# Kernel tuning notes

Measured on AMD Instinct MI355X. Metric: run time of the kernel, lower is better.

## Reference

```python
import jax, jax.numpy as jnp
import numpy as np


def _hard_sigmoid(x):
    # Keras ConvLSTM2D default recurrent_activation
    return jnp.clip(0.2 * x + 0.5, 0.0, 1.0)


def _conv_same(x, w):
    # x: [B,H,W,Cin], w: [kh,kw,Cin,Cout]
    return jax.lax.conv_general_dilated(
        x, w, window_strides=(1, 1), padding='SAME',
        dimension_numbers=('NHWC', 'HWIO', 'NHWC'))


def setup_inputs() -> dict:
    key = jax.random.key(0)
    ks = jax.random.split(key, 6)
    B, T, H, W, F = 16, 16, 64, 64, 64
    return {
        'inputs': jax.random.normal(ks[0], (B, T, H, W, 1), jnp.float32),  # only T is used
        'h0': jax.random.normal(ks[1], (B, H, W, F), jnp.float32),
        'c0': jax.random.normal(ks[2], (B, H, W, F), jnp.float32),
        'kernels': jax.random.normal(ks[3], (T, 3, 3, F, 4 * F), jnp.float32) * 0.05,
        'rec_kernels': jax.random.normal(ks[4], (T, 3, 3, F, 4 * F), jnp.float32) * 0.05,
        'bias': jnp.zeros((T, 4 * F), jnp.float32),
    }


def reference(inputs, h0, c0, kernels, rec_kernels, bias):
    # The layer feeds h back as the cell input each step, so the cell input x == h.
    # By linearity, conv(h, Wk) + conv(h, Uk) == conv(h, Wk + Uk); we fuse the two convs.
    # Gate order (Keras ConvLSTM2DCell): i, f, c, o.
    def step(carry, params):
        h, c = carry
        Wk, Uk, b = params  # [3,3,F,4F], [3,3,F,4F], [4F]
        z = _conv_same(h, Wk + Uk) + b  # [B,H,W,4F]
        zi, zf, zc, zo = jnp.split(z, 4, axis=-1)
        i = _hard_sigmoid(zi)
        f = _hard_sigmoid(zf)
        c_new = f * c + i * jnp.tanh(zc)
        o = _hard_sigmoid(zo)
        h_new = o * jnp.tanh(c_new)
        return (h_new, c_new), h_new

    (_, _), hs = jax.lax.scan(step, (h0, c0), (kernels, rec_kernels, bias))
    return jnp.moveaxis(hs, 0, 1)  # [B, T, H, W, F]
```

## Files before the change

### kernel.cpp

```cpp
#include <hip/hip_runtime.h>
#include <math.h>

typedef _Float16 f16;
typedef _Float16 f16x4 __attribute__((ext_vector_type(4)));
typedef _Float16 f16x8 __attribute__((ext_vector_type(8)));
typedef float f32x4 __attribute__((ext_vector_type(4)));

#define NB 16
#define NT 16
#define NH 64
#define NW 64
#define NF 64
#define NG 256
#define HWF ((size_t)NH * NW * NF)
#define OUT_BSTRIDE ((size_t)NT * HWF)
#define RS2 8448
#define WSTEP ((size_t)18432)

#define MFMA(a, b, c) __builtin_amdgcn_mfma_f32_16x16x32_f16((a), (b), (c), 0, 0, 0)

__device__ __forceinline__ void gload_lds16(const void* g, void* l) {
    __builtin_amdgcn_global_load_lds(
        (const __attribute__((address_space(1))) unsigned int*)(g),
        (__attribute__((address_space(3))) unsigned int*)(l), 16, 0, 0);
}

__device__ __forceinline__ float hsig(float x) {
    return fminf(fmaxf(0.2f * x + 0.5f, 0.0f), 1.0f);
}

__device__ __forceinline__ float ftanh(float x) {
    float t = __builtin_amdgcn_exp2f(x * 2.885390081777927f);
    return 1.0f - 2.0f * __builtin_amdgcn_rcpf(t + 1.0f);
}

__global__ void fuse_w_hi(const float* __restrict__ k, const float* __restrict__ rk,
                          f16* __restrict__ wf2) {
    int idx = blockIdx.x * 256 + threadIdx.x;
    if (idx >= NT * 9 * NG * 8) return;
    int g8   = idx & 7;
    int cout = (idx >> 3) & 255;
    int tt   = idx >> 11;
    int tap  = tt % 9;
    int t    = tt / 9;
    int kk = g8 >> 2, lg = g8 & 3;

    const float* ks = k  + (size_t)tt * NF * NG + cout;
    const float* rs = rk + (size_t)tt * NF * NG + cout;

    f16 hi8[8];
#pragma unroll
    for (int j = 0; j < 8; ++j) {
        int cin = kk * 32 + lg * 8 + j;
        hi8[j] = (f16)(ks[(size_t)cin * NG] + rs[(size_t)cin * NG]);
    }
    const int lane = lg * 16 + (cout & 15);
    const int cb   = ((cout >> 4) & 3) * 4 + (cout >> 6);
    size_t chunk = (size_t)t * WSTEP + (size_t)(tap * 2 + kk) * 1024 +
                   (size_t)cb * 64 + lane;
    *(f16x8*)&wf2[chunk * 8] = *(f16x8*)hi8;
}

__global__ void f32_to_f16(const float* __restrict__ src, f16* __restrict__ dst, int n4) {
    int i = blockIdx.x * 256 + threadIdx.x;
    if (i >= n4) return;
    float4 v = ((const float4*)src)[i];
    f16x4 o = { (f16)v.x, (f16)v.y, (f16)v.z, (f16)v.w };
    *(f16x4*)&dst[(size_t)i * 4] = o;
}

__global__ void __launch_bounds__(512, 4)
convlstm_mfma_step(const f16* __restrict__ h2in, f16* __restrict__ h2out,
                   f16* __restrict__ cbuf,
                   float* __restrict__ hout,
                   const f16* __restrict__ wt,
                   const float* __restrict__ bias)
{
    __shared__ __align__(16) unsigned char lds[4 * RS2];

    const int tid  = threadIdx.x;
    const int w    = tid >> 6;
    const int lane = tid & 63;

    const int id = blockIdx.x;
    const int bb = ((id & 7) << 1) + ((id >> 8) & 1);
    const int y0 = ((id >> 3) & 31) * 2;

    const int wm = w >> 2;
    const int wn = w & 3;
    const int lm = lane & 15;
    const int lg = lane >> 4;

    const f16x8* wb = (const f16x8*)wt + (size_t)(wn * 4) * 64 + lane;
    f16x8 bh[4];
#pragma unroll
    for (int nf = 0; nf < 4; ++nf)
        bh[nf] = wb[nf * 64];

    if (tid < 64) {
        int row = tid >> 4, side = (tid >> 3) & 1, j = tid & 7;
        *(f16x8*)&lds[row * RS2 + side * (65 * 128) + j * 16] = (f16x8)(_Float16)0.0f;
    }

    {
        const int r    = w >> 1;
        const int gy   = y0 - 1 + r;
        const int half = w & 1;
        const unsigned dbase = r * RS2 + 128 + half * 4096;
        if (gy >= 0 && gy < NH) {
            const unsigned char* gsrc = (const unsigned char*)h2in +
                ((((size_t)bb * NH + gy) * NW) << 7);
#pragma unroll
            for (int i = 0; i < 4; ++i) {
                const int xrel = half * 32 + i * 8 + (lane >> 3);
                const unsigned src = ((unsigned)xrel << 7) +
                    ((unsigned)((lane & 7) ^ ((xrel + 1) & 7)) << 4);
                gload_lds16(gsrc + src, (void*)&lds[dbase + i * 1024]);
            }
        } else {
            const f16x8 zf = (f16x8)(_Float16)0.0f;
#pragma unroll
            for (int i = 0; i < 4; ++i)
                *(f16x8*)&lds[dbase + i * 1024 + lane * 16] = zf;
        }
    }
    __syncthreads();

    f32x4 acc[4][4];
#pragma unroll
    for (int mf = 0; mf < 4; ++mf)
#pragma unroll
        for (int nf = 0; nf < 4; ++nf) acc[mf][nf] = (f32x4)0.0f;

    unsigned av[3][2];
#pragma unroll
    for (int d = 0; d < 3; ++d)
#pragma unroll
        for (int kk = 0; kk < 2; ++kk) {
            const int tx = lm + d;
            av[d][kk] = (unsigned)(tx * 128 +
                        (((kk * 4 + lg) ^ (tx & 7)) << 4));
        }

#pragma unroll
    for (int it = 0; it < 18; ++it) {
        if (it > 0) {
#pragma unroll
            for (int nf = 0; nf < 4; ++nf)
                bh[nf] = wb[(size_t)it * 1024 + nf * 64];
        }
        const int tap = it >> 1, kk = it & 1;
        const int ty = tap / 3;
        const int d  = tap - ty * 3;
        const unsigned abase = (unsigned)((wm + ty) * RS2) + av[d][kk];
        __builtin_amdgcn_s_setprio(1);
#pragma unroll
        for (int mf = 0; mf < 4; ++mf) {
            const f16x8 ah = *(const f16x8*)&lds[abase + mf * 2048];
#pragma unroll
            for (int nf = 0; nf < 4; ++nf)
                acc[mf][nf] = MFMA(ah, bh[nf], acc[mf][nf]);
        }
        __builtin_amdgcn_s_setprio(0);
    }

    const int f  = wn * 16 + lm;
    const int gy = y0 + wm;
    const float b0 = bias[f], b1 = bias[64 + f], b2 = bias[128 + f], b3 = bias[192 + f];

#pragma unroll
    for (int mf = 0; mf < 4; ++mf) {
        const int xb = mf * 16 + lg * 4;
        const size_t base = ((((size_t)bb * NH + gy) * NW + xb) << 6) + f;
        f16 cp4[4];
#pragma unroll
        for (int j = 0; j < 4; ++j)
            cp4[j] = cbuf[base + (size_t)j * 64];
#pragma unroll
        for (int j = 0; j < 4; ++j) {
            const float zi  = acc[mf][0][j] + b0;
            const float zfv = acc[mf][1][j] + b1;
            const float zc  = acc[mf][2][j] + b2;
            const float zo  = acc[mf][3][j] + b3;
            const float ig = hsig(zi), fg = hsig(zfv), og = hsig(zo);
            const float cn = fg * (float)cp4[j] + ig * ftanh(zc);
            cbuf[base + (size_t)j * 64] = (f16)cn;
            const float hn = og * ftanh(cn);
            hout[(size_t)bb * OUT_BSTRIDE + (((size_t)gy * NW + xb + j) << 6) + f] = hn;
            h2out[base + (size_t)j * 64] = (f16)hn;
        }
    }
}

extern "C" void kernel_launch(void* const* d_in, const int* in_sizes, int n_in,
                              void* d_out, int out_size, void* d_ws, size_t ws_size,
                              hipStream_t stream) {
    const float* h0    = (const float*)d_in[1];
    const float* c0    = (const float*)d_in[2];
    const float* kern  = (const float*)d_in[3];
    const float* rkern = (const float*)d_in[4];
    const float* bias  = (const float*)d_in[5];
    float* out = (float*)d_out;

    f16* wf2   = (f16*)d_ws;
    f16* h2a   = wf2 + (size_t)NT * WSTEP * 8;
    f16* h2b   = h2a + (size_t)NB * HWF;
    f16* cbuf  = h2b + (size_t)NB * HWF;

    const int n4 = (int)(NB * HWF / 4);
    fuse_w_hi<<<(NT * 9 * NG * 8 + 255) / 256, 256, 0, stream>>>(kern, rkern, wf2);
    f32_to_f16<<<(n4 + 255) / 256, 256, 0, stream>>>(h0, h2a, n4);
    f32_to_f16<<<(n4 + 255) / 256, 256, 0, stream>>>(c0, cbuf, n4);

    for (int t = 0; t < NT; ++t) {
        const f16* hin = (t & 1) ? h2b : h2a;
        f16* hnx       = (t & 1) ? h2a : h2b;
        convlstm_mfma_step<<<dim3(512), 512, 0, stream>>>(
            hin, hnx, cbuf,
            out + (size_t)t * HWF,
            wf2 + (size_t)t * WSTEP * 8,
            bias + t * NG);
    }
}
```

Measured before the change: 384.3 us.

## Enlarge block tile to four output rows and prefetch cell state early

Each block now computes four image rows instead of two, so each wave handles 8 M-fragments and reuses every loaded weight fragment across twice as many MFMAs. This halves the grid to 256 blocks, which reduces weight reloads and halo overhead (6 LDS rows per 4 outputs instead of 4 per 2). The cell-state values are loaded at kernel start so their latency overlaps the convolution. In exchange register pressure roughly doubles (launch bounds drop to 2 waves/SIMD), and the 256-block grid gives fewer blocks than before to spread across the CUs.

```diff
diff --git a/kernel.cpp b/kernel.cpp
--- a/kernel.cpp
+++ b/kernel.cpp
@@ -69,22 +69,22 @@
     *(f16x4*)&dst[(size_t)i * 4] = o;
 }
 
-__global__ void __launch_bounds__(512, 4)
+__global__ void __launch_bounds__(512, 2)
 convlstm_mfma_step(const f16* __restrict__ h2in, f16* __restrict__ h2out,
                    f16* __restrict__ cbuf,
                    float* __restrict__ hout,
                    const f16* __restrict__ wt,
                    const float* __restrict__ bias)
 {
-    __shared__ __align__(16) unsigned char lds[4 * RS2];
+    __shared__ __align__(16) unsigned char lds[6 * RS2];
 
     const int tid  = threadIdx.x;
     const int w    = tid >> 6;
     const int lane = tid & 63;
 
     const int id = blockIdx.x;
-    const int bb = ((id & 7) << 1) + ((id >> 8) & 1);
-    const int y0 = ((id >> 3) & 31) * 2;
+    const int bb = ((id & 7) << 1) + ((id >> 7) & 1);
+    const int y0 = ((id >> 3) & 15) * 4;
 
     const int wm = w >> 2;
     const int wn = w & 3;
@@ -97,38 +97,46 @@
     for (int nf = 0; nf < 4; ++nf)
         bh[nf] = wb[nf * 64];
 
-    if (tid < 64) {
+    const int f = wn * 16 + lm;
+    f16 cp[8][4];
+#pragma unroll
+    for (int mf = 0; mf < 8; ++mf) {
+        const int gy = y0 + wm * 2 + (mf >> 2);
+        const int xb = (mf & 3) * 16 + lg * 4;
+        const size_t base = ((((size_t)bb * NH + gy) * NW + xb) << 6) + f;
+#pragma unroll
+        for (int j = 0; j < 4; ++j)
+            cp[mf][j] = cbuf[base + (size_t)j * 64];
+    }
+
+    if (tid < 96) {
         int row = tid >> 4, side = (tid >> 3) & 1, j = tid & 7;
         *(f16x8*)&lds[row * RS2 + side * (65 * 128) + j * 16] = (f16x8)(_Float16)0.0f;
     }
 
     {
-        const int r    = w >> 1;
-        const int gy   = y0 - 1 + r;
-        const int half = w & 1;
-        const unsigned dbase = r * RS2 + 128 + half * 4096;
-        if (gy >= 0 && gy < NH) {
-            const unsigned char* gsrc = (const unsigned char*)h2in +
-                ((((size_t)bb * NH + gy) * NW) << 7);
-#pragma unroll
-            for (int i = 0; i < 4; ++i) {
-                const int xrel = half * 32 + i * 8 + (lane >> 3);
-                const unsigned src = ((unsigned)xrel << 7) +
-                    ((unsigned)((lane & 7) ^ ((xrel + 1) & 7)) << 4);
-                gload_lds16(gsrc + src, (void*)&lds[dbase + i * 1024]);
+        const int x = w * 8 + (lane >> 3);
+        const int g = lane & 7;
+        const unsigned src = ((unsigned)x << 7) +
+                             ((unsigned)(g ^ ((x + 1) & 7)) << 4);
+#pragma unroll
+        for (int k = 0; k < 6; ++k) {
+            const int gy = y0 - 1 + k;
+            const unsigned dbase = k * RS2 + 128 + w * 1024;
+            if (gy >= 0 && gy < NH) {
+                const unsigned char* gsrc = (const unsigned char*)h2in +
+                    ((((size_t)bb * NH + gy) * NW) << 7);
+                gload_lds16(gsrc + src, (void*)&lds[dbase]);
+            } else {
+                *(f16x8*)&lds[dbase + lane * 16] = (f16x8)(_Float16)0.0f;
             }
-        } else {
-            const f16x8 zf = (f16x8)(_Float16)0.0f;
-#pragma unroll
-            for (int i = 0; i < 4; ++i)
-                *(f16x8*)&lds[dbase + i * 1024 + lane * 16] = zf;
         }
     }
     __syncthreads();
 
-    f32x4 acc[4][4];
-#pragma unroll
-    for (int mf = 0; mf < 4; ++mf)
+    f32x4 acc[8][4];
+#pragma unroll
+    for (int mf = 0; mf < 8; ++mf)
 #pragma unroll
         for (int nf = 0; nf < 4; ++nf) acc[mf][nf] = (f32x4)0.0f;
 
@@ -152,11 +160,12 @@
         const int tap = it >> 1, kk = it & 1;
         const int ty = tap / 3;
         const int d  = tap - ty * 3;
-        const unsigned abase = (unsigned)((wm + ty) * RS2) + av[d][kk];
+        const unsigned abase = (unsigned)((wm * 2 + ty) * RS2) + av[d][kk];
         __builtin_amdgcn_s_setprio(1);
 #pragma unroll
-        for (int mf = 0; mf < 4; ++mf) {
-            const f16x8 ah = *(const f16x8*)&lds[abase + mf * 2048];
+        for (int mf = 0; mf < 8; ++mf) {
+            const f16x8 ah = *(const f16x8*)&lds[abase + (mf >> 2) * RS2 +
+                                                 (mf & 3) * 2048];
 #pragma unroll
             for (int nf = 0; nf < 4; ++nf)
                 acc[mf][nf] = MFMA(ah, bh[nf], acc[mf][nf]);
@@ -164,18 +173,13 @@
         __builtin_amdgcn_s_setprio(0);
     }
 
-    const int f  = wn * 16 + lm;
-    const int gy = y0 + wm;
     const float b0 = bias[f], b1 = bias[64 + f], b2 = bias[128 + f], b3 = bias[192 + f];
 
 #pragma unroll
-    for (int mf = 0; mf < 4; ++mf) {
-        const int xb = mf * 16 + lg * 4;
+    for (int mf = 0; mf < 8; ++mf) {
+        const int gy = y0 + wm * 2 + (mf >> 2);
+        const int xb = (mf & 3) * 16 + lg * 4;
         const size_t base = ((((size_t)bb * NH + gy) * NW + xb) << 6) + f;
-        f16 cp4[4];
-#pragma unroll
-        for (int j = 0; j < 4; ++j)
-            cp4[j] = cbuf[base + (size_t)j * 64];
 #pragma unroll
         for (int j = 0; j < 4; ++j) {
             const float zi  = acc[mf][0][j] + b0;
@@ -183,7 +187,7 @@
             const float zc  = acc[mf][2][j] + b2;
             const float zo  = acc[mf][3][j] + b3;
             const float ig = hsig(zi), fg = hsig(zfv), og = hsig(zo);
-            const float cn = fg * (float)cp4[j] + ig * ftanh(zc);
+            const float cn = fg * (float)cp[mf][j] + ig * ftanh(zc);
             cbuf[base + (size_t)j * 64] = (f16)cn;
             const float hn = og * ftanh(cn);
             hout[(size_t)bb * OUT_BSTRIDE + (((size_t)gy * NW + xb + j) << 6) + f] = hn;
@@ -215,7 +219,7 @@
     for (int t = 0; t < NT; ++t) {
         const f16* hin = (t & 1) ? h2b : h2a;
         f16* hnx       = (t & 1) ? h2a : h2b;
-        convlstm_mfma_step<<<dim3(512), 512, 0, stream>>>(
+        convlstm_mfma_step<<<dim3(256), 512, 0, stream>>>(
             hin, hnx, cbuf,
             out + (size_t)t * HWF,
             wf2 + (size_t)t * WSTEP * 8,
```

Result: no change. 378.8 us (-1.4%).
